# Kernel tuning notes

Measured on AMD Instinct MI355X. Metric: run time of the kernel, lower is better.

## Reference

```python
import jax, jax.numpy as jnp
import numpy as np

C, G, S, L, B = 16, 8192, 8, 3, 32


def setup_inputs() -> dict:
    key = jax.random.key(0)
    kx, kI = jax.random.split(key)
    # x: valuation vector over G ground atoms per batch element, in [0,1)
    x = jax.random.uniform(kx, (B, G), dtype=jnp.float32)
    # I: precomputed index tensor [C, G, S, L], indices into the G axis of x
    I = jax.random.randint(kI, (C, G, S, L), 0, G, dtype=jnp.int64)
    return {"x": x, "I": I}


def reference(x, I):
    # Equivalent of: for each clause i, gather(V_tild, 1, I_i) -> prod over L -> sum over S
    # torch gather semantics: out[b, g, s, l] = x[b, I[i, g, s, l]]
    # Vectorized over all clauses at once; no repeat/broadcast materialization beyond the gather.
    gathered = x[:, I]                        # [B, C, G, S, L]
    body = jnp.prod(gathered, axis=-1)        # conjunction over L body literals -> [B, C, G, S]
    clause_val = jnp.sum(body, axis=-1)       # sum over S substitutions -> [B, C, G]
    # torch.stack over clauses puts C first: [C, B, G]
    return jnp.transpose(clause_val, (1, 0, 2))
```

## Files before the change

kernel.cpp:

```cpp
#include <hip/hip_runtime.h>
#include <hip/hip_fp16.h>
#include <stdint.h>

#define Cc 16
#define Gg 8192
#define Ss 8
#define Ll 3
#define Bb 32

#define ZS 4
#define THREADS 512
#define ITERS 2

__global__ __launch_bounds__(256) void build_xh(const float* __restrict__ x,
                                                uint4* __restrict__ xh) {
    int t = blockIdx.x * 256 + threadIdx.x;
    int z = t >> 13;
    int g = t & (Gg - 1);
    uint32_t d[4];
    #pragma unroll
    for (int j = 0; j < 4; ++j) {
        __half2 h = __floats2half2_rn(x[(size_t)(8 * z + 2 * j) * Gg + g],
                                      x[(size_t)(8 * z + 2 * j + 1) * Gg + g]);
        d[j] = *(const uint32_t*)&h;
    }
    uint32_t s = (g >> 3) & 1u;
    xh[t] = s ? make_uint4(d[2], d[3], d[0], d[1])
              : make_uint4(d[0], d[1], d[2], d[3]);
}

__device__ __forceinline__ void clause_eval(const uint2* __restrict__ xl2,
                                            const int4 q[6], float acc[8]) {
    int idx[Ss * Ll] = {q[0].x, q[0].y, q[0].z, q[0].w, q[1].x, q[1].y, q[1].z, q[1].w,
                        q[2].x, q[2].y, q[2].z, q[2].w, q[3].x, q[3].y, q[3].z, q[3].w,
                        q[4].x, q[4].y, q[4].z, q[4].w, q[5].x, q[5].y, q[5].z, q[5].w};
    uint2 r0[Ss * Ll], r1[Ss * Ll];
    #pragma unroll
    for (int k = 0; k < Ss * Ll; ++k) {
        uint32_t u = (uint32_t)idx[k];
        uint32_t a0 = (u << 1) | ((u >> 3) & 1u);
        r0[k] = xl2[a0];
        r1[k] = xl2[a0 ^ 1u];
    }
    #pragma unroll
    for (int s = 0; s < Ss; ++s) {
        const int k0 = 3 * s, k1 = 3 * s + 1, k2 = 3 * s + 2;
        const uint32_t pa[4] = {r0[k0].x, r0[k0].y, r1[k0].x, r1[k0].y};
        const uint32_t pb[4] = {r0[k1].x, r0[k1].y, r1[k1].x, r1[k1].y};
        const uint32_t pd[4] = {r0[k2].x, r0[k2].y, r1[k2].x, r1[k2].y};
        #pragma unroll
        for (int j = 0; j < 4; ++j) {
            __half2 a = *(const __half2*)&pa[j];
            __half2 b = *(const __half2*)&pb[j];
            __half2 d = *(const __half2*)&pd[j];
            __half2 p = __hmul2(__hmul2(a, b), d);
            float2 pf = __half22float2(p);
            acc[2 * j] += pf.x;
            acc[2 * j + 1] += pf.y;
        }
    }
}

__global__ __launch_bounds__(THREADS) void clause_f16(const uint4* __restrict__ xh,
                                                      const int* __restrict__ I,
                                                      float* __restrict__ out) {
    __shared__ uint4 xl[Gg];
    const int tid = threadIdx.x;
    const int z = blockIdx.y;
    const int c = blockIdx.x >> 3;
    const int gbase = (blockIdx.x & 7) * (THREADS * ITERS);

    {
        const uint4* gs = xh + (size_t)z * Gg;
        uint4 t0[8];
        #pragma unroll
        for (int i = 0; i < 8; ++i) t0[i] = gs[tid + i * THREADS];
        #pragma unroll
        for (int i = 0; i < 8; ++i) xl[tid + i * THREADS] = t0[i];
        uint4 t1[8];
        #pragma unroll
        for (int i = 0; i < 8; ++i) t1[i] = gs[tid + (8 + i) * THREADS];
        #pragma unroll
        for (int i = 0; i < 8; ++i) xl[tid + (8 + i) * THREADS] = t1[i];
    }

    const int g0 = gbase + tid;
    const int g1 = gbase + THREADS + tid;
    const int4* ip0 = (const int4*)(I + ((size_t)c * Gg + g0) * (Ss * Ll));
    const int4* ip1 = (const int4*)(I + ((size_t)c * Gg + g1) * (Ss * Ll));
    int4 q0[6], q1[6];
    #pragma unroll
    for (int k = 0; k < 6; ++k) q0[k] = ip0[k];
    #pragma unroll
    for (int k = 0; k < 6; ++k) q1[k] = ip1[k];

    __syncthreads();

    const uint2* xl2 = (const uint2*)xl;
    float* opb = out + ((size_t)(c * Bb + 8 * z)) * Gg;

    {
        float acc[8] = {0, 0, 0, 0, 0, 0, 0, 0};
        clause_eval(xl2, q0, acc);
        #pragma unroll
        for (int j = 0; j < 8; ++j)
            opb[(size_t)j * Gg + g0] = acc[j];
    }
    {
        float acc[8] = {0, 0, 0, 0, 0, 0, 0, 0};
        clause_eval(xl2, q1, acc);
        #pragma unroll
        for (int j = 0; j < 8; ++j)
            opb[(size_t)j * Gg + g1] = acc[j];
    }
}

__global__ __launch_bounds__(256) void clause_kernel_direct(const float* __restrict__ x,
                                                            const int* __restrict__ I,
                                                            float* __restrict__ out) {
    const int tid = threadIdx.x;
    const int b = tid & 31;
    const int j = tid >> 5;
    const int g = blockIdx.x * 8 + j;
    const int c = blockIdx.y;

    const int* Icg = I + (size_t)(c * Gg + g) * (Ss * Ll);
    float sum = 0.f;
    #pragma unroll
    for (int s = 0; s < Ss; ++s) {
        float p0 = x[(size_t)b * Gg + Icg[3 * s + 0]];
        float p1 = x[(size_t)b * Gg + Icg[3 * s + 1]];
        float p2 = x[(size_t)b * Gg + Icg[3 * s + 2]];
        sum += p0 * p1 * p2;
    }
    out[(size_t)(c * Bb + b) * Gg + g] = sum;
}

extern "C" void kernel_launch(void* const* d_in, const int* in_sizes, int n_in,
                              void* d_out, int out_size, void* d_ws, size_t ws_size,
                              hipStream_t stream) {
    const float* x = (const float*)d_in[0];
    const int* I = (const int*)d_in[1];
    float* out = (float*)d_out;

    const size_t xh_bytes = (size_t)ZS * Gg * sizeof(uint4);

    if (ws_size >= xh_bytes) {
        uint4* xh = (uint4*)d_ws;
        build_xh<<<(ZS * Gg) / 256, 256, 0, stream>>>(x, xh);
        clause_f16<<<dim3((Cc * Gg) / (THREADS * ITERS), ZS), THREADS, 0, stream>>>(xh, I, out);
    } else {
        clause_kernel_direct<<<dim3(Gg / 8, Cc), 256, 0, stream>>>(x, I, out);
    }
}
```

Baseline: 83.34 us.

## Fuse fp16 x-table build into clause kernel with 1024-thread blocks

Removes the separate build_xh pre-pass and workspace buffer: each block now converts its 8-batch slice of x to packed half2 directly into shared memory, after issuing the index loads. Blocks grow to 1024 threads, the grid becomes 1-D with a block-index remap, and the per-thread gather is split into two halves to reduce register pressure. This saves one launch and a global round trip. In exchange, every block redundantly reads 8x8192 floats of x, and the larger blocks plus the occupancy hint of 4 may limit residency.

```diff
diff --git a/kernel.cpp b/kernel.cpp
--- a/kernel.cpp
+++ b/kernel.cpp
@@ -9,80 +9,57 @@
 #define Bb 32
 
 #define ZS 4
-#define THREADS 512
+#define THREADS 1024
 #define ITERS 2
-
-__global__ __launch_bounds__(256) void build_xh(const float* __restrict__ x,
-                                                uint4* __restrict__ xh) {
-    int t = blockIdx.x * 256 + threadIdx.x;
-    int z = t >> 13;
-    int g = t & (Gg - 1);
-    uint32_t d[4];
-    #pragma unroll
-    for (int j = 0; j < 4; ++j) {
-        __half2 h = __floats2half2_rn(x[(size_t)(8 * z + 2 * j) * Gg + g],
-                                      x[(size_t)(8 * z + 2 * j + 1) * Gg + g]);
-        d[j] = *(const uint32_t*)&h;
-    }
-    uint32_t s = (g >> 3) & 1u;
-    xh[t] = s ? make_uint4(d[2], d[3], d[0], d[1])
-              : make_uint4(d[0], d[1], d[2], d[3]);
-}
 
 __device__ __forceinline__ void clause_eval(const uint2* __restrict__ xl2,
                                             const int4 q[6], float acc[8]) {
-    int idx[Ss * Ll] = {q[0].x, q[0].y, q[0].z, q[0].w, q[1].x, q[1].y, q[1].z, q[1].w,
-                        q[2].x, q[2].y, q[2].z, q[2].w, q[3].x, q[3].y, q[3].z, q[3].w,
-                        q[4].x, q[4].y, q[4].z, q[4].w, q[5].x, q[5].y, q[5].z, q[5].w};
-    uint2 r0[Ss * Ll], r1[Ss * Ll];
     #pragma unroll
-    for (int k = 0; k < Ss * Ll; ++k) {
-        uint32_t u = (uint32_t)idx[k];
-        uint32_t a0 = (u << 1) | ((u >> 3) & 1u);
-        r0[k] = xl2[a0];
-        r1[k] = xl2[a0 ^ 1u];
-    }
-    #pragma unroll
-    for (int s = 0; s < Ss; ++s) {
-        const int k0 = 3 * s, k1 = 3 * s + 1, k2 = 3 * s + 2;
-        const uint32_t pa[4] = {r0[k0].x, r0[k0].y, r1[k0].x, r1[k0].y};
-        const uint32_t pb[4] = {r0[k1].x, r0[k1].y, r1[k1].x, r1[k1].y};
-        const uint32_t pd[4] = {r0[k2].x, r0[k2].y, r1[k2].x, r1[k2].y};
+    for (int h = 0; h < 2; ++h) {
+        const int4 qa = q[3 * h + 0];
+        const int4 qb = q[3 * h + 1];
+        const int4 qc = q[3 * h + 2];
+        int idx[12] = {qa.x, qa.y, qa.z, qa.w,
+                       qb.x, qb.y, qb.z, qb.w,
+                       qc.x, qc.y, qc.z, qc.w};
+        uint2 r0[12], r1[12];
         #pragma unroll
-        for (int j = 0; j < 4; ++j) {
-            __half2 a = *(const __half2*)&pa[j];
-            __half2 b = *(const __half2*)&pb[j];
-            __half2 d = *(const __half2*)&pd[j];
-            __half2 p = __hmul2(__hmul2(a, b), d);
-            float2 pf = __half22float2(p);
-            acc[2 * j] += pf.x;
-            acc[2 * j + 1] += pf.y;
+        for (int k = 0; k < 12; ++k) {
+            uint32_t u = (uint32_t)idx[k];
+            uint32_t a0 = (u << 1) | ((u >> 3) & 1u);
+            r0[k] = xl2[a0];
+            r1[k] = xl2[a0 ^ 1u];
+        }
+        #pragma unroll
+        for (int s = 0; s < 4; ++s) {
+            const int k0 = 3 * s, k1 = 3 * s + 1, k2 = 3 * s + 2;
+            const uint32_t pa[4] = {r0[k0].x, r0[k0].y, r1[k0].x, r1[k0].y};
+            const uint32_t pb[4] = {r0[k1].x, r0[k1].y, r1[k1].x, r1[k1].y};
+            const uint32_t pd[4] = {r0[k2].x, r0[k2].y, r1[k2].x, r1[k2].y};
+            #pragma unroll
+            for (int j = 0; j < 4; ++j) {
+                __half2 a = *(const __half2*)&pa[j];
+                __half2 b = *(const __half2*)&pb[j];
+                __half2 d = *(const __half2*)&pd[j];
+                __half2 p = __hmul2(__hmul2(a, b), d);
+                float2 pf = __half22float2(p);
+                acc[2 * j]     += pf.x;
+                acc[2 * j + 1] += pf.y;
+            }
         }
     }
 }
 
-__global__ __launch_bounds__(THREADS) void clause_f16(const uint4* __restrict__ xh,
-                                                      const int* __restrict__ I,
-                                                      float* __restrict__ out) {
+__global__ __launch_bounds__(THREADS, 4) void clause_f16_fused(
+        const float* __restrict__ x, const int* __restrict__ I,
+        float* __restrict__ out) {
     __shared__ uint4 xl[Gg];
     const int tid = threadIdx.x;
-    const int z = blockIdx.y;
-    const int c = blockIdx.x >> 3;
-    const int gbase = (blockIdx.x & 7) * (THREADS * ITERS);
 
-    {
-        const uint4* gs = xh + (size_t)z * Gg;
-        uint4 t0[8];
-        #pragma unroll
-        for (int i = 0; i < 8; ++i) t0[i] = gs[tid + i * THREADS];
-        #pragma unroll
-        for (int i = 0; i < 8; ++i) xl[tid + i * THREADS] = t0[i];
-        uint4 t1[8];
-        #pragma unroll
-        for (int i = 0; i < 8; ++i) t1[i] = gs[tid + (8 + i) * THREADS];
-        #pragma unroll
-        for (int i = 0; i < 8; ++i) xl[tid + (8 + i) * THREADS] = t1[i];
-    }
+    const int lb = (blockIdx.x & 7) * 32 + (blockIdx.x >> 3);
+    const int c = lb >> 4;
+    const int z = (lb >> 2) & 3;
+    const int gbase = (lb & 3) * (THREADS * ITERS);
 
     const int g0 = gbase + tid;
     const int g1 = gbase + THREADS + tid;
@@ -93,6 +70,26 @@
     for (int k = 0; k < 6; ++k) q0[k] = ip0[k];
     #pragma unroll
     for (int k = 0; k < 6; ++k) q1[k] = ip1[k];
+
+    {
+        const float* xs = x + (size_t)(8 * z) * Gg;
+        #pragma unroll 4
+        for (int k = 0; k < 8; ++k) {
+            const int g = tid + k * THREADS;
+            float v[8];
+            #pragma unroll
+            for (int b = 0; b < 8; ++b) v[b] = xs[(size_t)b * Gg + g];
+            uint32_t d[4];
+            #pragma unroll
+            for (int j = 0; j < 4; ++j) {
+                __half2 h = __floats2half2_rn(v[2 * j], v[2 * j + 1]);
+                d[j] = *(const uint32_t*)&h;
+            }
+            const uint32_t s = (g >> 3) & 1u;
+            xl[g] = s ? make_uint4(d[2], d[3], d[0], d[1])
+                      : make_uint4(d[0], d[1], d[2], d[3]);
+        }
+    }
 
     __syncthreads();
 
@@ -115,41 +112,14 @@
     }
 }
 
-__global__ __launch_bounds__(256) void clause_kernel_direct(const float* __restrict__ x,
-                                                            const int* __restrict__ I,
-                                                            float* __restrict__ out) {
-    const int tid = threadIdx.x;
-    const int b = tid & 31;
-    const int j = tid >> 5;
-    const int g = blockIdx.x * 8 + j;
-    const int c = blockIdx.y;
-
-    const int* Icg = I + (size_t)(c * Gg + g) * (Ss * Ll);
-    float sum = 0.f;
-    #pragma unroll
-    for (int s = 0; s < Ss; ++s) {
-        float p0 = x[(size_t)b * Gg + Icg[3 * s + 0]];
-        float p1 = x[(size_t)b * Gg + Icg[3 * s + 1]];
-        float p2 = x[(size_t)b * Gg + Icg[3 * s + 2]];
-        sum += p0 * p1 * p2;
-    }
-    out[(size_t)(c * Bb + b) * Gg + g] = sum;
-}
-
 extern "C" void kernel_launch(void* const* d_in, const int* in_sizes, int n_in,
                               void* d_out, int out_size, void* d_ws, size_t ws_size,
                               hipStream_t stream) {
     const float* x = (const float*)d_in[0];
     const int* I = (const int*)d_in[1];
     float* out = (float*)d_out;
+    (void)d_ws; (void)ws_size;
 
-    const size_t xh_bytes = (size_t)ZS * Gg * sizeof(uint4);
-
-    if (ws_size >= xh_bytes) {
-        uint4* xh = (uint4*)d_ws;
-        build_xh<<<(ZS * Gg) / 256, 256, 0, stream>>>(x, xh);
-        clause_f16<<<dim3((Cc * Gg) / (THREADS * ITERS), ZS), THREADS, 0, stream>>>(xh, I, out);
-    } else {
-        clause_kernel_direct<<<dim3(Gg / 8, Cc), 256, 0, stream>>>(x, I, out);
-    }
+    const int grid = (Cc * Gg * ZS) / (THREADS * ITERS);
+    clause_f16_fused<<<grid, THREADS, 0, stream>>>(x, I, out);
 }
```

New measurement: 80.74 us. 3.1% less time.
